# Kernel optimization log

Hardware: AMD Instinct MI355X
Metric: run time of the kernel (lower is better)

Reference implementation:

```python
import jax, jax.numpy as jnp
import numpy as np

# dims: batch, tokens, channels, heads, head_dim, slices, context_slices, context_dim
B, N, C, H, D, G, SC, DC = 2, 32768, 256, 8, 32, 32, 64, 32
EPS_SLICE = 1e-5


def _ln(x, g, b):
    m = x.mean(-1, keepdims=True)
    v = ((x - m) ** 2).mean(-1, keepdims=True)
    return (x - m) * jax.lax.rsqrt(v + 1e-5) * g + b


def setup_inputs() -> dict:
    key = jax.random.key(0)
    ks = jax.random.split(key, 16)
    w = lambda k, s: jax.random.normal(k, s, jnp.float32) * 0.02
    return dict(
        fx=jax.random.normal(ks[0], (B, N, C), jnp.float32),
        context=jax.random.normal(ks[1], (B, H, SC, DC), jnp.float32),
        ln1_g=jnp.ones((C,), jnp.float32), ln1_b=jnp.zeros((C,), jnp.float32),
        Wfx=w(ks[2], (C, H * D)), bfx=jnp.zeros((H * D,), jnp.float32),
        Wx=w(ks[3], (C, H * D)), bx=jnp.zeros((H * D,), jnp.float32),
        Wslice=w(ks[4], (D, G)), bslice=jnp.zeros((G,), jnp.float32),
        temperature=0.5 * jnp.ones((1, H, 1, 1), jnp.float32),
        Wq=w(ks[5], (D, D)), Wk=w(ks[6], (D, D)), Wv=w(ks[7], (D, D)),
        Wcq=w(ks[8], (D, D)), bcq=jnp.zeros((D,), jnp.float32),
        Wck=w(ks[9], (DC, D)), bck=jnp.zeros((D,), jnp.float32),
        Wcv=w(ks[10], (DC, D)), bcv=jnp.zeros((D,), jnp.float32),
        state_mixing=jnp.zeros((), jnp.float32),
        Wout=w(ks[11], (H * D, C)), bout=jnp.zeros((C,), jnp.float32),
        ln2_g=jnp.ones((C,), jnp.float32), ln2_b=jnp.zeros((C,), jnp.float32),
        Wm1=w(ks[12], (C, 4 * C)), bm1=jnp.zeros((4 * C,), jnp.float32),
        Wm2=w(ks[13], (4 * C, C)), bm2=jnp.zeros((C,), jnp.float32),
    )


def reference(fx, context, ln1_g, ln1_b, Wfx, bfx, Wx, bx, Wslice, bslice,
              temperature, Wq, Wk, Wv, Wcq, bcq, Wck, bck, Wcv, bcv,
              state_mixing, Wout, bout, ln2_g, ln2_b, Wm1, bm1, Wm2, bm2):
    # --- GALE attention on pre-normed input (Transolver physics attention + cross) ---
    x = _ln(fx, ln1_g, ln1_b)
    fxm = (x @ Wfx + bfx).reshape(B, N, H, D).transpose(0, 2, 1, 3)  # b h n d
    xm = (x @ Wx + bx).reshape(B, N, H, D).transpose(0, 2, 1, 3)    # b h n d
    # slice weights: softmax over slices with learnable per-head temperature
    sw = jax.nn.softmax((xm @ Wslice + bslice) / temperature, axis=-1)  # b h n g
    norm = sw.sum(2)  # b h g
    st = jnp.einsum('bhnd,bhng->bhgd', fxm, sw) / (norm + EPS_SLICE)[..., None]
    scale = D ** -0.5
    # self-attention among slice tokens (no bias on q/k/v)
    q, k, v = st @ Wq, st @ Wk, st @ Wv
    sattn = jax.nn.softmax(jnp.einsum('bhgd,bhmd->bhgm', q, k) * scale, axis=-1)
    self_tok = jnp.einsum('bhgm,bhmd->bhgd', sattn, v)
    # cross-attention of slice tokens onto geometry/global context
    cq = st @ Wcq + bcq
    ck = context @ Wck + bck
    cv = context @ Wcv + bcv
    cattn = jax.nn.softmax(jnp.einsum('bhgd,bhsd->bhgs', cq, ck) * scale, axis=-1)
    cross_tok = jnp.einsum('bhgs,bhsd->bhgd', cattn, cv)
    # sigmoid-gated mix
    mw = jax.nn.sigmoid(state_mixing)
    ost = mw * self_tok + (1.0 - mw) * cross_tok
    # de-slice back to tokens and output-project
    out = jnp.einsum('bhgd,bhng->bhnd', ost, sw)
    out = out.transpose(0, 2, 1, 3).reshape(B, N, H * D) @ Wout + bout
    fx = fx + out  # residual 1
    # --- MLP block ---
    h = _ln(fx, ln2_g, ln2_b)
    fx = fx + (jax.nn.gelu(h @ Wm1 + bm1, approximate=False) @ Wm2 + bm2)
    return fx
```

## Files before the change

kernel.cpp:

```cpp
#include <hip/hip_runtime.h>
#include <hip/hip_bf16.h>

#define BATCH 2
#define NTOK  32768
#define CH    256
#define NH    8
#define HDIM  32
#define NG    32
#define NSC   64
#define NDC   32

typedef __attribute__((ext_vector_type(8))) short short8v;
typedef __attribute__((ext_vector_type(4))) short short4v;
typedef __attribute__((ext_vector_type(4))) float f32x4;

static __device__ __forceinline__ short f2bf(float f) {
    __hip_bfloat16 h = __float2bfloat16(f);
    return __builtin_bit_cast(short, h);
}
static __device__ __forceinline__ float bf2f(short s) {
    return __bfloat162float(__builtin_bit_cast(__hip_bfloat16, s));
}

__global__ __launch_bounds__(256) void kconv_transpose(
    const float* __restrict__ in, __hip_bfloat16* __restrict__ out,
    int K, int N)
{
    __shared__ float t[32][33];
    const int nb = N >> 5;
    const int bk = blockIdx.x / nb;
    const int bn = blockIdx.x % nb;
    const int c = threadIdx.x & 31, r0 = threadIdx.x >> 5;
    #pragma unroll
    for (int i = 0; i < 4; ++i) {
        const int r = r0 + i * 8;
        t[r][c] = in[(long)(bk * 32 + r) * N + bn * 32 + c];
    }
    __syncthreads();
    #pragma unroll
    for (int i = 0; i < 4; ++i) {
        const int r = r0 + i * 8;
        out[(long)(bn * 32 + r) * K + bk * 32 + c] = __float2bfloat16(t[c][r]);
    }
}

__global__ __launch_bounds__(256) void kcomb(
    const float* __restrict__ Wx, const float* __restrict__ bx,
    const float* __restrict__ Wsl, const float* __restrict__ bsl,
    __hip_bfloat16* __restrict__ wcat2, float* __restrict__ bcomb)
{
    __shared__ float wcol[32];
    const int hc = blockIdx.x;
    const int h = hc >> 5, g = hc & 31;
    const int tid = threadIdx.x;
    if (tid < 32) wcol[tid] = Wsl[tid * 32 + g];
    __syncthreads();
    float a = 0.f;
    #pragma unroll
    for (int d = 0; d < 32; ++d) a += Wx[tid * 256 + h * 32 + d] * wcol[d];
    wcat2[(long)hc * 256 + tid] = __float2bfloat16(a);
    if (tid == 0) {
        float s = bsl[g];
        #pragma unroll
        for (int d = 0; d < 32; ++d) s += bx[h * 32 + d] * wcol[d];
        bcomb[hc] = s;
    }
}

__global__ __launch_bounds__(256, 2) void k1_mfma(
    const float* __restrict__ fx,
    const float* __restrict__ g1, const float* __restrict__ b1,
    const __hip_bfloat16* __restrict__ wcat,
    const float* __restrict__ bfx, const float* __restrict__ bcomb,
    const float* __restrict__ temp,
    __hip_bfloat16* __restrict__ fxm_o, __hip_bfloat16* __restrict__ sw_o)
{
    __shared__ __align__(16) char lds[65536];
    const int tid = threadIdx.x;
    const int lane = tid & 63, wid = tid >> 6;
    const long tok0 = (long)blockIdx.x * 64;
    const int col = lane & 15, kq = lane >> 4;
    const int swz = (col & 7) << 4;
    const int ep = ((kq * 16) ^ swz) & 48;
    const int e0 = (swz & 64) | ep;
    const int e1 = ((swz & 64) ^ 64) | ep;
    const int ab0 = col * 512 + e0, ab1 = col * 512 + e1;

    {
        const float4 gv = *reinterpret_cast<const float4*>(g1 + lane * 4);
        const float4 bv = *reinterpret_cast<const float4*>(b1 + lane * 4);
        for (int tt = 0; tt < 16; ++tt) {
            const int r = wid * 16 + tt;
            const float4 v = *reinterpret_cast<const float4*>(fx + (tok0 + r) * 256 + lane * 4);
            float s = v.x + v.y + v.z + v.w;
            float s2 = v.x * v.x + v.y * v.y + v.z * v.z + v.w * v.w;
            #pragma unroll
            for (int off = 32; off; off >>= 1) {
                s  += __shfl_xor(s,  off);
                s2 += __shfl_xor(s2, off);
            }
            const float mean = s * (1.f / 256.f);
            const float rs = rsqrtf(s2 * (1.f / 256.f) - mean * mean + 1e-5f);
            short4v o;
            o[0] = f2bf((v.x - mean) * rs * gv.x + bv.x);
            o[1] = f2bf((v.y - mean) * rs * gv.y + bv.y);
            o[2] = f2bf((v.z - mean) * rs * gv.z + bv.z);
            o[3] = f2bf((v.w - mean) * rs * gv.w + bv.w);
            const int addr = r * 512 + ((lane * 8) ^ ((r & 7) << 4));
            *reinterpret_cast<short4v*>(lds + addr) = o;
        }
    }
    __syncthreads();

    f32x4 acc[4][8];
    #pragma unroll
    for (int mt = 0; mt < 4; ++mt)
        #pragma unroll
        for (int nt = 0; nt < 8; ++nt) acc[mt][nt] = (f32x4){0.f, 0.f, 0.f, 0.f};

    const short* wp = reinterpret_cast<const short*>(wcat) + (wid * 128 + col) * 256 + kq * 8;
    #pragma unroll 2
    for (int j = 0; j < 4; ++j) {
        short8v a0[4], a1[4];
        #pragma unroll
        for (int mt = 0; mt < 4; ++mt) {
            a0[mt] = *reinterpret_cast<const short8v*>(lds + mt * 8192 + j * 128 + ab0);
            a1[mt] = *reinterpret_cast<const short8v*>(lds + mt * 8192 + j * 128 + ab1);
        }
        #pragma unroll
        for (int nt = 0; nt < 8; ++nt) {
            const short8v b0 = *reinterpret_cast<const short8v*>(wp + nt * 4096 + j * 64);
            const short8v b1 = *reinterpret_cast<const short8v*>(wp + nt * 4096 + j * 64 + 32);
            #pragma unroll
            for (int mt = 0; mt < 4; ++mt) {
                acc[mt][nt] = __builtin_amdgcn_mfma_f32_16x16x32_bf16(a0[mt], b0, acc[mt][nt], 0, 0, 0);
                acc[mt][nt] = __builtin_amdgcn_mfma_f32_16x16x32_bf16(a1[mt], b1, acc[mt][nt], 0, 0, 0);
            }
        }
    }
    __syncthreads();

    #pragma unroll
    for (int nt = 0; nt < 8; ++nt) {
        const int c = wid * 128 + nt * 16 + col;
        const float bb = (c < 256) ? bfx[c] : bcomb[c - 256];
        #pragma unroll
        for (int mt = 0; mt < 4; ++mt) {
            #pragma unroll
            for (int r = 0; r < 4; ++r) {
                const int row = mt * 16 + kq * 4 + r;
                const int byte = row * 1024 + ((c * 2) ^ ((row & 7) << 4));
                *reinterpret_cast<short*>(lds + byte) = f2bf(acc[mt][nt][r] + bb);
            }
        }
    }
    __syncthreads();

    #pragma unroll
    for (int it = 0; it < 8; ++it) {
        const int idx = it * 256 + tid;
        const int row = idx >> 5, ch = idx & 31;
        const short8v val = *reinterpret_cast<const short8v*>(
            lds + row * 1024 + ((ch * 16) ^ ((row & 7) << 4)));
        *reinterpret_cast<short8v*>(
            reinterpret_cast<short*>(fxm_o) + (tok0 + row) * 256 + ch * 8) = val;
    }

    #pragma unroll
    for (int pp = 0; pp < 2; ++pp) {
        const int p = pp * 256 + tid;
        const int t = p >> 3, h = p & 7;
        const float it_ = 1.f / temp[h];
        float lg[32];
        #pragma unroll
        for (int g = 0; g < 32; ++g) {
            const int byte = t * 1024 + (((256 + h * 32 + g) * 2) ^ ((t & 7) << 4));
            lg[g] = bf2f(*reinterpret_cast<const short*>(lds + byte)) * it_;
        }
        float mx = -1e30f;
        #pragma unroll
        for (int g = 0; g < 32; ++g) mx = fmaxf(mx, lg[g]);
        float ssum = 0.f;
        #pragma unroll
        for (int g = 0; g < 32; ++g) { lg[g] = __expf(lg[g] - mx); ssum += lg[g]; }
        const float inv = 1.f / ssum;
        #pragma unroll
        for (int g = 0; g < 32; ++g) {
            const int byte = t * 1024 + (((256 + h * 32 + g) * 2) ^ ((t & 7) << 4));
            *reinterpret_cast<short*>(lds + byte) = f2bf(lg[g] * inv);
        }
    }
    __syncthreads();

    #pragma unroll
    for (int it = 0; it < 8; ++it) {
        const int idx = it * 256 + tid;
        const int row = idx >> 5, ch = idx & 31;
        const short8v val = *reinterpret_cast<const short8v*>(
            lds + row * 1024 + ((512 + ch * 16) ^ ((row & 7) << 4)));
        *reinterpret_cast<short8v*>(
            reinterpret_cast<short*>(sw_o) + (tok0 + row) * 256 + ch * 8) = val;
    }
}

__global__ __launch_bounds__(256) void k2_st_partial(
    const __hip_bfloat16* __restrict__ fxm, const __hip_bfloat16* __restrict__ sw,
    float* __restrict__ pst, float* __restrict__ pn)
{
    __shared__ float fl[32][32];
    __shared__ float sl[32][32];
    const int tid = threadIdx.x;
    const int blk = blockIdx.x;
    const int bh = blk >> 5, chunk = blk & 31;
    const int b = bh >> 3, h = bh & 7;
    const long nbase = (long)b * NTOK + (long)chunk * 1024;
    const int g = tid >> 3, dq = tid & 7, db = dq * 4;
    const int lr = tid >> 3, lc4 = (tid & 7) * 4;
    float a0 = 0.f, a1 = 0.f, a2 = 0.f, a3 = 0.f, nacc = 0.f;

    for (int nb = 0; nb < 1024; nb += 32) {
        const long base = (nbase + nb + lr) * 256 + h * 32 + lc4;
        const short4v fv = *reinterpret_cast<const short4v*>(
            reinterpret_cast<const short*>(fxm) + base);
        const short4v sv = *reinterpret_cast<const short4v*>(
            reinterpret_cast<const short*>(sw) + base);
        float4 ff, sf;
        ff.x = bf2f(fv[0]); ff.y = bf2f(fv[1]); ff.z = bf2f(fv[2]); ff.w = bf2f(fv[3]);
        sf.x = bf2f(sv[0]); sf.y = bf2f(sv[1]); sf.z = bf2f(sv[2]); sf.w = bf2f(sv[3]);
        __syncthreads();
        *reinterpret_cast<float4*>(&fl[lr][lc4]) = ff;
        *reinterpret_cast<float4*>(&sl[lr][lc4]) = sf;
        __syncthreads();
        #pragma unroll
        for (int t = 0; t < 32; ++t) {
            const float s = sl[t][g];
            if (dq == 0) nacc += s;
            a0 += s * fl[t][db + 0];
            a1 += s * fl[t][db + 1];
            a2 += s * fl[t][db + 2];
            a3 += s * fl[t][db + 3];
        }
    }
    float* o = pst + (long)blk * 1024 + g * 32 + db;
    o[0] = a0; o[1] = a1; o[2] = a2; o[3] = a3;
    if (dq == 0) pn[blk * 32 + g] = nacc;
}

__global__ __launch_bounds__(256) void k3_slice_attn(
    const float* __restrict__ pst, const float* __restrict__ pn,
    const float* __restrict__ ctx,
    const float* __restrict__ Wq, const float* __restrict__ Wk, const float* __restrict__ Wv,
    const float* __restrict__ Wcq, const float* __restrict__ bcq,
    const float* __restrict__ Wck, const float* __restrict__ bck,
    const float* __restrict__ Wcv, const float* __restrict__ bcv,
    const float* __restrict__ mix, __hip_bfloat16* __restrict__ ostT_o)
{
    __shared__ float st[1024], qm[1024], km[1024], vm[1024], cqm[1024];
    __shared__ float ckm[2048], cvm[2048], attn[2048], stok[1024], nb[32];
    const int tid = threadIdx.x;
    const int bh = blockIdx.x;

    if (tid < 32) {
        float s = 0.f;
        for (int c = 0; c < 32; ++c) s += pn[(bh * 32 + c) * 32 + tid];
        nb[tid] = s;
    }
    __syncthreads();
    for (int i = tid; i < 1024; i += 256) {
        float s = 0.f;
        for (int c = 0; c < 32; ++c) s += pst[(long)(bh * 32 + c) * 1024 + i];
        st[i] = s / (nb[i >> 5] + 1e-5f);
    }
    __syncthreads();

    for (int i = tid; i < 1024; i += 256) {
        const int g = i >> 5, d = i & 31;
        float aq = 0.f, ak = 0.f, av = 0.f, ac = bcq[d];
        #pragma unroll
        for (int e = 0; e < 32; ++e) {
            const float s = st[g * 32 + e];
            aq += s * Wq[e * 32 + d];
            ak += s * Wk[e * 32 + d];
            av += s * Wv[e * 32 + d];
            ac += s * Wcq[e * 32 + d];
        }
        qm[i] = aq; km[i] = ak; vm[i] = av; cqm[i] = ac;
    }
    const float* cbp = ctx + (long)bh * (NSC * NDC);
    for (int i = tid; i < 2048; i += 256) {
        const int s_ = i >> 5, d = i & 31;
        float w1 = bck[d], w2 = bcv[d];
        #pragma unroll
        for (int e = 0; e < 32; ++e) {
            const float cval = cbp[s_ * 32 + e];
            w1 += cval * Wck[e * 32 + d];
            w2 += cval * Wcv[e * 32 + d];
        }
        ckm[i] = w1; cvm[i] = w2;
    }
    __syncthreads();

    const float scale = 0.17677669529663687f;
    for (int i = tid; i < 1024; i += 256) {
        const int g = i >> 5, m = i & 31;
        float a = 0.f;
        #pragma unroll
        for (int d = 0; d < 32; ++d) a += qm[g * 32 + d] * km[m * 32 + d];
        attn[i] = a * scale;
    }
    __syncthreads();
    if (tid < 32) {
        float mx = -1e30f;
        for (int m = 0; m < 32; ++m) mx = fmaxf(mx, attn[tid * 32 + m]);
        float s = 0.f;
        for (int m = 0; m < 32; ++m) { const float e = expf(attn[tid * 32 + m] - mx); attn[tid * 32 + m] = e; s += e; }
        const float inv = 1.f / s;
        for (int m = 0; m < 32; ++m) attn[tid * 32 + m] *= inv;
    }
    __syncthreads();
    for (int i = tid; i < 1024; i += 256) {
        const int g = i >> 5, d = i & 31;
        float a = 0.f;
        #pragma unroll
        for (int m = 0; m < 32; ++m) a += attn[g * 32 + m] * vm[m * 32 + d];
        stok[i] = a;
    }
    __syncthreads();
    for (int i = tid; i < 2048; i += 256) {
        const int g = i >> 6, s_ = i & 63;
        float a = 0.f;
        #pragma unroll
        for (int d = 0; d < 32; ++d) a += cqm[g * 32 + d] * ckm[s_ * 32 + d];
        attn[i] = a * scale;
    }
    __syncthreads();
    if (tid < 32) {
        float mx = -1e30f;
        for (int m = 0; m < 64; ++m) mx = fmaxf(mx, attn[tid * 64 + m]);
        float s = 0.f;
        for (int m = 0; m < 64; ++m) { const float e = expf(attn[tid * 64 + m] - mx); attn[tid * 64 + m] = e; s += e; }
        const float inv = 1.f / s;
        for (int m = 0; m < 64; ++m) attn[tid * 64 + m] *= inv;
    }
    __syncthreads();
    const float mw = 1.f / (1.f + expf(-mix[0]));
    for (int i = tid; i < 1024; i += 256) {
        const int g = i >> 5, d = i & 31;
        float a = 0.f;
        #pragma unroll
        for (int s_ = 0; s_ < 64; ++s_) a += attn[g * 64 + s_] * cvm[s_ * 32 + d];
        const float val = mw * stok[i] + (1.f - mw) * a;
        ostT_o[(long)bh * 1024 + d * 32 + g] = __float2bfloat16(val);
    }
}

__global__ __launch_bounds__(256, 2) void k4_mfma(
    const __hip_bfloat16* __restrict__ sw, const __hip_bfloat16* __restrict__ ostT,
    const __hip_bfloat16* __restrict__ woutt, const float* __restrict__ bout,
    const float* __restrict__ fx, float* __restrict__ out)
{
    __shared__ __align__(16) char lds[65536];
    const int tid = threadIdx.x;
    const int lane = tid & 63, wid = tid >> 6;
    const long tok0 = (long)blockIdx.x * 64;
    const int b = (int)(tok0 >> 15);
    const int col = lane & 15, kq = lane >> 4;
    const int swz = (col & 7) << 4;
    const int ep = ((kq * 16) ^ swz) & 48;
    const int e0 = (swz & 64) | ep;
    const int e1 = ((swz & 64) ^ 64) | ep;
    const int ab0 = col * 512 + e0, ab1 = col * 512 + e1;

    #pragma unroll
    for (int it = 0; it < 8; ++it) {
        const int idx = it * 256 + tid;
        const int row = idx >> 5, ch = idx & 31;
        const short8v val = *reinterpret_cast<const short8v*>(
            reinterpret_cast<const short*>(sw) + (tok0 + row) * 256 + ch * 8);
        *reinterpret_cast<short8v*>(lds + row * 512 + ((ch * 16) ^ ((row & 7) << 4))) = val;
    }
    __syncthreads();

    f32x4 accal[2][4][2];
    #pragma unroll
    for (int hh = 0; hh < 2; ++hh) {
        const int h = wid * 2 + hh;
        short8v a[4];
        #pragma unroll
        for (int mt = 0; mt < 4; ++mt)
            a[mt] = *reinterpret_cast<const short8v*>(
                lds + mt * 8192 + wid * 128 + (hh ? ab1 : ab0));
        #pragma unroll
        for (int nt = 0; nt < 2; ++nt) {
            const int d = nt * 16 + col;
            const short8v bfr = *reinterpret_cast<const short8v*>(
                reinterpret_cast<const short*>(ostT) + ((b * 8 + h) * 32 + d) * 32 + kq * 8);
            #pragma unroll
            for (int mt = 0; mt < 4; ++mt) {
                accal[hh][mt][nt] = (f32x4){0.f, 0.f, 0.f, 0.f};
                accal[hh][mt][nt] = __builtin_amdgcn_mfma_f32_16x16x32_bf16(
                    a[mt], bfr, accal[hh][mt][nt], 0, 0, 0);
            }
        }
    }
    #pragma unroll
    for (int hh = 0; hh < 2; ++hh) {
        const int h = wid * 2 + hh;
        #pragma unroll
        for (int nt = 0; nt < 2; ++nt) {
            const int cc = h * 32 + nt * 16 + col;
            #pragma unroll
            for (int mt = 0; mt < 4; ++mt) {
                #pragma unroll
                for (int r = 0; r < 4; ++r) {
                    const int row = mt * 16 + kq * 4 + r;
                    const int byte = 32768 + row * 512 + ((cc * 2) ^ ((row & 7) << 4));
                    *reinterpret_cast<short*>(lds + byte) = f2bf(accal[hh][mt][nt][r]);
                }
            }
        }
    }
    __syncthreads();

    f32x4 acc[4][4];
    #pragma unroll
    for (int mt = 0; mt < 4; ++mt)
        #pragma unroll
        for (int nt = 0; nt < 4; ++nt) acc[mt][nt] = (f32x4){0.f, 0.f, 0.f, 0.f};

    const short* wp = reinterpret_cast<const short*>(woutt) + (wid * 64 + col) * 256 + kq * 8;
    #pragma unroll 2
    for (int j = 0; j < 4; ++j) {
        short8v a0[4], a1[4];
        #pragma unroll
        for (int mt = 0; mt < 4; ++mt) {
            a0[mt] = *reinterpret_cast<const short8v*>(lds + 32768 + mt * 8192 + j * 128 + ab0);
            a1[mt] = *reinterpret_cast<const short8v*>(lds + 32768 + mt * 8192 + j * 128 + ab1);
        }
        #pragma unroll
        for (int nt = 0; nt < 4; ++nt) {
            const short8v b0 = *reinterpret_cast<const short8v*>(wp + nt * 4096 + j * 64);
            const short8v b1 = *reinterpret_cast<const short8v*>(wp + nt * 4096 + j * 64 + 32);
            #pragma unroll
            for (int mt = 0; mt < 4; ++mt) {
                acc[mt][nt] = __builtin_amdgcn_mfma_f32_16x16x32_bf16(a0[mt], b0, acc[mt][nt], 0, 0, 0);
                acc[mt][nt] = __builtin_amdgcn_mfma_f32_16x16x32_bf16(a1[mt], b1, acc[mt][nt], 0, 0, 0);
            }
        }
    }

    #pragma unroll
    for (int nt = 0; nt < 4; ++nt) {
        const int c = wid * 64 + nt * 16 + col;
        const float bb = bout[c];
        #pragma unroll
        for (int mt = 0; mt < 4; ++mt) {
            #pragma unroll
            for (int r = 0; r < 4; ++r) {
                const int row = mt * 16 + kq * 4 + r;
                const long idx = (tok0 + row) * 256 + c;
                out[idx] = acc[mt][nt][r] + bb + fx[idx];
            }
        }
    }
}

__global__ __launch_bounds__(512, 4) void k5_mlp_mfma(
    float* __restrict__ io,
    const float* __restrict__ g2, const float* __restrict__ b2,
    const __hip_bfloat16* __restrict__ w1t, const float* __restrict__ bm1,
    const __hip_bfloat16* __restrict__ w2t, const float* __restrict__ bm2)
{
    __shared__ __align__(16) char lds[65536];
    const int tid = threadIdx.x;
    const int lane = tid & 63, wid = tid >> 6;
    const long tok0 = (long)blockIdx.x * 64;
    const int col = lane & 15, kq = lane >> 4;
    const int n0 = wid * 32;
    const int swz = (col & 7) << 4;
    const int ep = ((kq * 16) ^ swz) & 48;
    const int e0 = (swz & 64) | ep;
    const int e1 = ((swz & 64) ^ 64) | ep;
    const int ab0 = col * 512 + e0, ab1 = col * 512 + e1;

    {
        const float4 gv = *reinterpret_cast<const float4*>(g2 + lane * 4);
        const float4 bv = *reinterpret_cast<const float4*>(b2 + lane * 4);
        #pragma unroll
        for (int tt = 0; tt < 8; ++tt) {
            const int r = wid * 8 + tt;
            const float4 v = *reinterpret_cast<const float4*>(io + (tok0 + r) * 256 + lane * 4);
            float s = v.x + v.y + v.z + v.w;
            float s2 = v.x * v.x + v.y * v.y + v.z * v.z + v.w * v.w;
            #pragma unroll
            for (int off = 32; off; off >>= 1) {
                s  += __shfl_xor(s,  off);
                s2 += __shfl_xor(s2, off);
            }
            const float mean = s * (1.f / 256.f);
            const float rs = rsqrtf(s2 * (1.f / 256.f) - mean * mean + 1e-5f);
            short4v o;
            o[0] = f2bf((v.x - mean) * rs * gv.x + bv.x);
            o[1] = f2bf((v.y - mean) * rs * gv.y + bv.y);
            o[2] = f2bf((v.z - mean) * rs * gv.z + bv.z);
            o[3] = f2bf((v.w - mean) * rs * gv.w + bv.w);
            const int addr = r * 512 + ((lane * 8) ^ ((r & 7) << 4));
            *reinterpret_cast<short4v*>(lds + addr) = o;
        }
    }
    __syncthreads();

    const short* w1s = reinterpret_cast<const short*>(w1t) + (n0 + col) * 256 + kq * 8;
    const short* w2s = reinterpret_cast<const short*>(w2t) + (n0 + col) * 1024 + kq * 8;
    const int gsw = (kq & 1) << 6;

    f32x4 accO[4][2];
    #pragma unroll
    for (int mt = 0; mt < 4; ++mt)
        #pragma unroll
        for (int nt = 0; nt < 2; ++nt) accO[mt][nt] = (f32x4){0.f, 0.f, 0.f, 0.f};

    for (int ch = 0; ch < 4; ++ch) {
        f32x4 accP[4][2];
        #pragma unroll
        for (int mt = 0; mt < 4; ++mt)
            #pragma unroll
            for (int nt = 0; nt < 2; ++nt) accP[mt][nt] = (f32x4){0.f, 0.f, 0.f, 0.f};

        #pragma unroll 2
        for (int j = 0; j < 4; ++j) {
            short8v a0[4], a1[4];
            #pragma unroll
            for (int mt = 0; mt < 4; ++mt) {
                a0[mt] = *reinterpret_cast<const short8v*>(lds + mt * 8192 + j * 128 + ab0);
                a1[mt] = *reinterpret_cast<const short8v*>(lds + mt * 8192 + j * 128 + ab1);
            }
            #pragma unroll
            for (int nt = 0; nt < 2; ++nt) {
                const short8v b0 = *reinterpret_cast<const short8v*>(
                    w1s + ch * 65536 + nt * 4096 + j * 64);
                const short8v b1 = *reinterpret_cast<const short8v*>(
                    w1s + ch * 65536 + nt * 4096 + j * 64 + 32);
                #pragma unroll
                for (int mt = 0; mt < 4; ++mt) {
                    accP[mt][nt] = __builtin_amdgcn_mfma_f32_16x16x32_bf16(a0[mt], b0, accP[mt][nt], 0, 0, 0);
                    accP[mt][nt] = __builtin_amdgcn_mfma_f32_16x16x32_bf16(a1[mt], b1, accP[mt][nt], 0, 0, 0);
                }
            }
        }

        __syncthreads();
        #pragma unroll
        for (int nt = 0; nt < 2; ++nt) {
            const float b1v = bm1[ch * 256 + n0 + nt * 16 + col];
            const int k2i2 = (n0 + nt * 16 + col) * 2;
            #pragma unroll
            for (int mt = 0; mt < 4; ++mt) {
                #pragma unroll
                for (int r = 0; r < 4; ++r) {
                    float m = accP[mt][nt][r] + b1v;
                    const float u = __builtin_fmaf(0.044715f * m, m * m, m);
                    const float e = __expf(-1.5957691216057308f * u);
                    m = m * __builtin_amdgcn_rcpf(1.f + e);
                    const int byte = 32768 + kq * 2048 + mt * 8192 + r * 512
                                     + (k2i2 ^ (gsw + r * 16));
                    *reinterpret_cast<short*>(lds + byte) = f2bf(m);
                }
            }
        }
        __syncthreads();

        #pragma unroll 2
        for (int j = 0; j < 4; ++j) {
            short8v a0[4], a1[4];
            #pragma unroll
            for (int mt = 0; mt < 4; ++mt) {
                a0[mt] = *reinterpret_cast<const short8v*>(lds + 32768 + mt * 8192 + j * 128 + ab0);
                a1[mt] = *reinterpret_cast<const short8v*>(lds + 32768 + mt * 8192 + j * 128 + ab1);
            }
            #pragma unroll
            for (int nt = 0; nt < 2; ++nt) {
                const short8v b0 = *reinterpret_cast<const short8v*>(
                    w2s + nt * 16384 + ch * 256 + j * 64);
                const short8v b1 = *reinterpret_cast<const short8v*>(
                    w2s + nt * 16384 + ch * 256 + j * 64 + 32);
                #pragma unroll
                for (int mt = 0; mt < 4; ++mt) {
                    accO[mt][nt] = __builtin_amdgcn_mfma_f32_16x16x32_bf16(a0[mt], b0, accO[mt][nt], 0, 0, 0);
                    accO[mt][nt] = __builtin_amdgcn_mfma_f32_16x16x32_bf16(a1[mt], b1, accO[mt][nt], 0, 0, 0);
                }
            }
        }
    }

    #pragma unroll
    for (int nt = 0; nt < 2; ++nt) {
        const int c = n0 + nt * 16 + col;
        const float b2v = bm2[c];
        #pragma unroll
        for (int mt = 0; mt < 4; ++mt) {
            #pragma unroll
            for (int r = 0; r < 4; ++r) {
                const int row = mt * 16 + kq * 4 + r;
                const long idx = (tok0 + row) * 256 + c;
                io[idx] = io[idx] + accO[mt][nt][r] + b2v;
            }
        }
    }
}

extern "C" void kernel_launch(void* const* d_in, const int* in_sizes, int n_in,
                              void* d_out, int out_size, void* d_ws, size_t ws_size,
                              hipStream_t stream)
{
    const float* fx   = (const float*)d_in[0];
    const float* ctx  = (const float*)d_in[1];
    const float* g1   = (const float*)d_in[2];
    const float* b1   = (const float*)d_in[3];
    const float* Wfx  = (const float*)d_in[4];
    const float* bfx  = (const float*)d_in[5];
    const float* Wx   = (const float*)d_in[6];
    const float* bx   = (const float*)d_in[7];
    const float* Wsl  = (const float*)d_in[8];
    const float* bsl  = (const float*)d_in[9];
    const float* temp = (const float*)d_in[10];
    const float* Wq   = (const float*)d_in[11];
    const float* Wk   = (const float*)d_in[12];
    const float* Wv   = (const float*)d_in[13];
    const float* Wcq  = (const float*)d_in[14];
    const float* bcq  = (const float*)d_in[15];
    const float* Wck  = (const float*)d_in[16];
    const float* bck  = (const float*)d_in[17];
    const float* Wcv  = (const float*)d_in[18];
    const float* bcv  = (const float*)d_in[19];
    const float* mix  = (const float*)d_in[20];
    const float* Wout = (const float*)d_in[21];
    const float* bout = (const float*)d_in[22];
    const float* g2   = (const float*)d_in[23];
    const float* b2   = (const float*)d_in[24];
    const float* Wm1  = (const float*)d_in[25];
    const float* bm1  = (const float*)d_in[26];
    const float* Wm2  = (const float*)d_in[27];
    const float* bm2  = (const float*)d_in[28];
    float* out = (float*)d_out;

    char* ws = (char*)d_ws;
    __hip_bfloat16* fxm  = (__hip_bfloat16*)ws;
    __hip_bfloat16* sw   = (__hip_bfloat16*)(ws + (size_t)33554432);
    float* pst = (float*)(ws + (size_t)67108864);
    float* pn  = (float*)(ws + (size_t)69206016);
    __hip_bfloat16* ostT  = (__hip_bfloat16*)(ws + (size_t)69271552);
    __hip_bfloat16* wcat  = (__hip_bfloat16*)(ws + (size_t)69304320);
    __hip_bfloat16* woutt = (__hip_bfloat16*)(ws + (size_t)69566464);
    __hip_bfloat16* w1t   = (__hip_bfloat16*)(ws + (size_t)69697536);
    __hip_bfloat16* w2t   = (__hip_bfloat16*)(ws + (size_t)70221824);
    float* bcomb          = (float*)(ws + (size_t)70746112);

    kconv_transpose<<<64,  256, 0, stream>>>(Wfx, wcat,  256, 256);
    kcomb<<<256, 256, 0, stream>>>(Wx, bx, Wsl, bsl, wcat + 65536, bcomb);
    kconv_transpose<<<64,  256, 0, stream>>>(Wout, woutt, 256, 256);
    kconv_transpose<<<256, 256, 0, stream>>>(Wm1, w1t,    256, 1024);
    kconv_transpose<<<256, 256, 0, stream>>>(Wm2, w2t,    1024, 256);

    k1_mfma<<<1024, 256, 0, stream>>>(fx, g1, b1, wcat, bfx, bcomb, temp,
                                      fxm, sw);
    k2_st_partial<<<512, 256, 0, stream>>>(fxm, sw, pst, pn);
    k3_slice_attn<<<16, 256, 0, stream>>>(pst, pn, ctx, Wq, Wk, Wv,
                                          Wcq, bcq, Wck, bck, Wcv, bcv, mix, ostT);
    k4_mfma<<<1024, 256, 0, stream>>>(sw, ostT, woutt, bout, fx, out);
    k5_mlp_mfma<<<1024, 512, 0, stream>>>(out, g2, b2, w1t, bm1, w2t, bm2);
}
```

Measured before the change: 334.7 us.

## Rewrite slice reduction, stage epilogues through LDS, software-pipeline MLP GEMMs

The slice-token reduction kernel now has each wave accumulate a 4x4 register tile over its own 256-token range with direct global loads, then combines the four waves' partials through shared memory. This removes the per-step double barrier and LDS round trip. The output-projection and MLP epilogues now stage results in LDS and write the residual add with coalesced float4 accesses instead of strided scalar global stores. The MLP loop is restructured so the second GEMM for chunk ch runs interleaved with the first GEMM for chunk ch+1, overlapping the two MFMA streams at the cost of more live accumulators and register pressure.

```diff
diff --git a/kernel.cpp b/kernel.cpp
--- a/kernel.cpp
+++ b/kernel.cpp
@@ -207,43 +207,57 @@
     const __hip_bfloat16* __restrict__ fxm, const __hip_bfloat16* __restrict__ sw,
     float* __restrict__ pst, float* __restrict__ pn)
 {
-    __shared__ float fl[32][32];
-    __shared__ float sl[32][32];
-    const int tid = threadIdx.x;
+    __shared__ float psum[4][32][32];
+    __shared__ float pns[4][32];
+    const int tid = threadIdx.x, wid = tid >> 6, lane = tid & 63;
     const int blk = blockIdx.x;
     const int bh = blk >> 5, chunk = blk & 31;
     const int b = bh >> 3, h = bh & 7;
-    const long nbase = (long)b * NTOK + (long)chunk * 1024;
-    const int g = tid >> 3, dq = tid & 7, db = dq * 4;
-    const int lr = tid >> 3, lc4 = (tid & 7) * 4;
-    float a0 = 0.f, a1 = 0.f, a2 = 0.f, a3 = 0.f, nacc = 0.f;
-
-    for (int nb = 0; nb < 1024; nb += 32) {
-        const long base = (nbase + nb + lr) * 256 + h * 32 + lc4;
-        const short4v fv = *reinterpret_cast<const short4v*>(
-            reinterpret_cast<const short*>(fxm) + base);
-        const short4v sv = *reinterpret_cast<const short4v*>(
-            reinterpret_cast<const short*>(sw) + base);
-        float4 ff, sf;
-        ff.x = bf2f(fv[0]); ff.y = bf2f(fv[1]); ff.z = bf2f(fv[2]); ff.w = bf2f(fv[3]);
-        sf.x = bf2f(sv[0]); sf.y = bf2f(sv[1]); sf.z = bf2f(sv[2]); sf.w = bf2f(sv[3]);
-        __syncthreads();
-        *reinterpret_cast<float4*>(&fl[lr][lc4]) = ff;
-        *reinterpret_cast<float4*>(&sl[lr][lc4]) = sf;
-        __syncthreads();
-        #pragma unroll
-        for (int t = 0; t < 32; ++t) {
-            const float s = sl[t][g];
-            if (dq == 0) nacc += s;
-            a0 += s * fl[t][db + 0];
-            a1 += s * fl[t][db + 1];
-            a2 += s * fl[t][db + 2];
-            a3 += s * fl[t][db + 3];
-        }
-    }
-    float* o = pst + (long)blk * 1024 + g * 32 + db;
-    o[0] = a0; o[1] = a1; o[2] = a2; o[3] = a3;
-    if (dq == 0) pn[blk * 32 + g] = nacc;
+    const long rbase = (long)b * NTOK + (long)chunk * 1024 + wid * 256;
+    const int gB = lane >> 3, dB = lane & 7;
+    const short* sp = reinterpret_cast<const short*>(sw) + rbase * 256 + h * 32 + gB * 4;
+    const short* fp = reinterpret_cast<const short*>(fxm) + rbase * 256 + h * 32 + dB * 4;
+
+    float acc[4][4];
+    float nacc[4];
+    #pragma unroll
+    for (int i = 0; i < 4; ++i) {
+        nacc[i] = 0.f;
+        #pragma unroll
+        for (int j = 0; j < 4; ++j) acc[i][j] = 0.f;
+    }
+
+    #pragma unroll 4
+    for (int r = 0; r < 256; ++r) {
+        const short4v s4 = *reinterpret_cast<const short4v*>(sp + r * 256);
+        const short4v f4 = *reinterpret_cast<const short4v*>(fp + r * 256);
+        float sg[4], fd[4];
+        #pragma unroll
+        for (int i = 0; i < 4; ++i) { sg[i] = bf2f(s4[i]); fd[i] = bf2f(f4[i]); }
+        #pragma unroll
+        for (int gg = 0; gg < 4; ++gg) {
+            nacc[gg] += sg[gg];
+            #pragma unroll
+            for (int dd = 0; dd < 4; ++dd) acc[gg][dd] += sg[gg] * fd[dd];
+        }
+    }
+
+    #pragma unroll
+    for (int gg = 0; gg < 4; ++gg) {
+        #pragma unroll
+        for (int dd = 0; dd < 4; ++dd)
+            psum[wid][gB * 4 + gg][dB * 4 + dd] = acc[gg][dd];
+        if (dB == 0) pns[wid][gB * 4 + gg] = nacc[gg];
+    }
+    __syncthreads();
+
+    for (int i = tid; i < 1024; i += 256) {
+        const int g = i >> 5, d = i & 31;
+        pst[(long)blk * 1024 + i] =
+            psum[0][g][d] + psum[1][g][d] + psum[2][g][d] + psum[3][g][d];
+    }
+    if (tid < 32)
+        pn[blk * 32 + tid] = pns[0][tid] + pns[1][tid] + pns[2][tid] + pns[3][tid];
 }
 
 __global__ __launch_bounds__(256) void k3_slice_attn(
@@ -449,6 +463,8 @@
         }
     }
 
+    __syncthreads();
+    float* lf = reinterpret_cast<float*>(lds);
     #pragma unroll
     for (int nt = 0; nt < 4; ++nt) {
         const int c = wid * 64 + nt * 16 + col;
@@ -458,10 +474,21 @@
             #pragma unroll
             for (int r = 0; r < 4; ++r) {
                 const int row = mt * 16 + kq * 4 + r;
-                const long idx = (tok0 + row) * 256 + c;
-                out[idx] = acc[mt][nt][r] + bb + fx[idx];
-            }
-        }
+                lf[row * 256 + c] = acc[mt][nt][r] + bb;
+            }
+        }
+    }
+    __syncthreads();
+    #pragma unroll
+    for (int it = 0; it < 16; ++it) {
+        const int q = it * 256 + tid;
+        const int row = q >> 6, c4 = (q & 63) * 4;
+        const float4 v = *reinterpret_cast<const float4*>(lf + row * 256 + c4);
+        const long gidx = (tok0 + row) * 256 + c4;
+        const float4 f = *reinterpret_cast<const float4*>(fx + gidx);
+        float4 o;
+        o.x = v.x + f.x; o.y = v.y + f.y; o.z = v.z + f.z; o.w = v.w + f.w;
+        *reinterpret_cast<float4*>(out + gidx) = o;
     }
 }
 
@@ -514,41 +541,36 @@
     const short* w2s = reinterpret_cast<const short*>(w2t) + (n0 + col) * 1024 + kq * 8;
     const int gsw = (kq & 1) << 6;
 
-    f32x4 accO[4][2];
+    f32x4 accP[4][2], accO[4][2];
     #pragma unroll
     for (int mt = 0; mt < 4; ++mt)
         #pragma unroll
-        for (int nt = 0; nt < 2; ++nt) accO[mt][nt] = (f32x4){0.f, 0.f, 0.f, 0.f};
+        for (int nt = 0; nt < 2; ++nt) {
+            accP[mt][nt] = (f32x4){0.f, 0.f, 0.f, 0.f};
+            accO[mt][nt] = (f32x4){0.f, 0.f, 0.f, 0.f};
+        }
+
+    #pragma unroll 1
+    for (int j = 0; j < 4; ++j) {
+        short8v b0[2], b1[2];
+        #pragma unroll
+        for (int nt = 0; nt < 2; ++nt) {
+            b0[nt] = *reinterpret_cast<const short8v*>(w1s + nt * 4096 + j * 64);
+            b1[nt] = *reinterpret_cast<const short8v*>(w1s + nt * 4096 + j * 64 + 32);
+        }
+        #pragma unroll
+        for (int mt = 0; mt < 4; ++mt) {
+            const short8v a0 = *reinterpret_cast<const short8v*>(lds + mt * 8192 + j * 128 + ab0);
+            const short8v a1 = *reinterpret_cast<const short8v*>(lds + mt * 8192 + j * 128 + ab1);
+            #pragma unroll
+            for (int nt = 0; nt < 2; ++nt) {
+                accP[mt][nt] = __builtin_amdgcn_mfma_f32_16x16x32_bf16(a0, b0[nt], accP[mt][nt], 0, 0, 0);
+                accP[mt][nt] = __builtin_amdgcn_mfma_f32_16x16x32_bf16(a1, b1[nt], accP[mt][nt], 0, 0, 0);
+            }
+        }
+    }
 
     for (int ch = 0; ch < 4; ++ch) {
-        f32x4 accP[4][2];
-        #pragma unroll
-        for (int mt = 0; mt < 4; ++mt)
-            #pragma unroll
-            for (int nt = 0; nt < 2; ++nt) accP[mt][nt] = (f32x4){0.f, 0.f, 0.f, 0.f};
-
-        #pragma unroll 2
-        for (int j = 0; j < 4; ++j) {
-            short8v a0[4], a1[4];
-            #pragma unroll
-            for (int mt = 0; mt < 4; ++mt) {
-                a0[mt] = *reinterpret_cast<const short8v*>(lds + mt * 8192 + j * 128 + ab0);
-                a1[mt] = *reinterpret_cast<const short8v*>(lds + mt * 8192 + j * 128 + ab1);
-            }
-            #pragma unroll
-            for (int nt = 0; nt < 2; ++nt) {
-                const short8v b0 = *reinterpret_cast<const short8v*>(
-                    w1s + ch * 65536 + nt * 4096 + j * 64);
-                const short8v b1 = *reinterpret_cast<const short8v*>(
-                    w1s + ch * 65536 + nt * 4096 + j * 64 + 32);
-                #pragma unroll
-                for (int mt = 0; mt < 4; ++mt) {
-                    accP[mt][nt] = __builtin_amdgcn_mfma_f32_16x16x32_bf16(a0[mt], b0, accP[mt][nt], 0, 0, 0);
-                    accP[mt][nt] = __builtin_amdgcn_mfma_f32_16x16x32_bf16(a1[mt], b1, accP[mt][nt], 0, 0, 0);
-                }
-            }
-        }
-
         __syncthreads();
         #pragma unroll
         for (int nt = 0; nt < 2; ++nt) {
@@ -570,42 +592,93 @@
         }
         __syncthreads();
 
-        #pragma unroll 2
-        for (int j = 0; j < 4; ++j) {
-            short8v a0[4], a1[4];
-            #pragma unroll
-            for (int mt = 0; mt < 4; ++mt) {
-                a0[mt] = *reinterpret_cast<const short8v*>(lds + 32768 + mt * 8192 + j * 128 + ab0);
-                a1[mt] = *reinterpret_cast<const short8v*>(lds + 32768 + mt * 8192 + j * 128 + ab1);
-            }
-            #pragma unroll
-            for (int nt = 0; nt < 2; ++nt) {
-                const short8v b0 = *reinterpret_cast<const short8v*>(
-                    w2s + nt * 16384 + ch * 256 + j * 64);
-                const short8v b1 = *reinterpret_cast<const short8v*>(
-                    w2s + nt * 16384 + ch * 256 + j * 64 + 32);
+        if (ch < 3) {
+            #pragma unroll
+            for (int mt = 0; mt < 4; ++mt)
+                #pragma unroll
+                for (int nt = 0; nt < 2; ++nt) accP[mt][nt] = (f32x4){0.f, 0.f, 0.f, 0.f};
+
+            #pragma unroll 1
+            for (int j = 0; j < 4; ++j) {
+                short8v b20[2], b21[2], b10[2], b11[2];
+                #pragma unroll
+                for (int nt = 0; nt < 2; ++nt) {
+                    b20[nt] = *reinterpret_cast<const short8v*>(w2s + nt * 16384 + ch * 256 + j * 64);
+                    b21[nt] = *reinterpret_cast<const short8v*>(w2s + nt * 16384 + ch * 256 + j * 64 + 32);
+                    b10[nt] = *reinterpret_cast<const short8v*>(w1s + (ch + 1) * 65536 + nt * 4096 + j * 64);
+                    b11[nt] = *reinterpret_cast<const short8v*>(w1s + (ch + 1) * 65536 + nt * 4096 + j * 64 + 32);
+                }
                 #pragma unroll
                 for (int mt = 0; mt < 4; ++mt) {
-                    accO[mt][nt] = __builtin_amdgcn_mfma_f32_16x16x32_bf16(a0[mt], b0, accO[mt][nt], 0, 0, 0);
-                    accO[mt][nt] = __builtin_amdgcn_mfma_f32_16x16x32_bf16(a1[mt], b1, accO[mt][nt], 0, 0, 0);
+                    const short8v x0 = *reinterpret_cast<const short8v*>(lds + 32768 + mt * 8192 + j * 128 + ab0);
+                    const short8v x1 = *reinterpret_cast<const short8v*>(lds + 32768 + mt * 8192 + j * 128 + ab1);
+                    const short8v y0 = *reinterpret_cast<const short8v*>(lds + mt * 8192 + j * 128 + ab0);
+                    const short8v y1 = *reinterpret_cast<const short8v*>(lds + mt * 8192 + j * 128 + ab1);
+                    #pragma unroll
+                    for (int nt = 0; nt < 2; ++nt) {
+                        accO[mt][nt] = __builtin_amdgcn_mfma_f32_16x16x32_bf16(x0, b20[nt], accO[mt][nt], 0, 0, 0);
+                        accO[mt][nt] = __builtin_amdgcn_mfma_f32_16x16x32_bf16(x1, b21[nt], accO[mt][nt], 0, 0, 0);
+                        accP[mt][nt] = __builtin_amdgcn_mfma_f32_16x16x32_bf16(y0, b10[nt], accP[mt][nt], 0, 0, 0);
+                        accP[mt][nt] = __builtin_amdgcn_mfma_f32_16x16x32_bf16(y1, b11[nt], accP[mt][nt], 0, 0, 0);
+                    }
                 }
             }
-        }
-    }
-
-    #pragma unroll
-    for (int nt = 0; nt < 2; ++nt) {
-        const int c = n0 + nt * 16 + col;
-        const float b2v = bm2[c];
-        #pragma unroll
-        for (int mt = 0; mt < 4; ++mt) {
-            #pragma unroll
-            for (int r = 0; r < 4; ++r) {
-                const int row = mt * 16 + kq * 4 + r;
-                const long idx = (tok0 + row) * 256 + c;
-                io[idx] = io[idx] + accO[mt][nt][r] + b2v;
-            }
-        }
+        } else {
+            #pragma unroll 1
+            for (int j = 0; j < 4; ++j) {
+                short8v b20[2], b21[2];
+                #pragma unroll
+                for (int nt = 0; nt < 2; ++nt) {
+                    b20[nt] = *reinterpret_cast<const short8v*>(w2s + nt * 16384 + 3 * 256 + j * 64);
+                    b21[nt] = *reinterpret_cast<const short8v*>(w2s + nt * 16384 + 3 * 256 + j * 64 + 32);
+                }
+                #pragma unroll
+                for (int mt = 0; mt < 4; ++mt) {
+                    const short8v x0 = *reinterpret_cast<const short8v*>(lds + 32768 + mt * 8192 + j * 128 + ab0);
+                    const short8v x1 = *reinterpret_cast<const short8v*>(lds + 32768 + mt * 8192 + j * 128 + ab1);
+                    #pragma unroll
+                    for (int nt = 0; nt < 2; ++nt) {
+                        accO[mt][nt] = __builtin_amdgcn_mfma_f32_16x16x32_bf16(x0, b20[nt], accO[mt][nt], 0, 0, 0);
+                        accO[mt][nt] = __builtin_amdgcn_mfma_f32_16x16x32_bf16(x1, b21[nt], accO[mt][nt], 0, 0, 0);
+                    }
+                }
+            }
+        }
+    }
+
+    __syncthreads();
+    float* lf = reinterpret_cast<float*>(lds);
+    #pragma unroll
+    for (int half = 0; half < 2; ++half) {
+        if ((wid >> 2) == half) {
+            #pragma unroll
+            for (int nt = 0; nt < 2; ++nt) {
+                const int c = n0 + nt * 16 + col;
+                const float b2v = bm2[c];
+                const int cl = c - half * 128;
+                #pragma unroll
+                for (int mt = 0; mt < 4; ++mt) {
+                    #pragma unroll
+                    for (int r = 0; r < 4; ++r) {
+                        const int row = mt * 16 + kq * 4 + r;
+                        lf[row * 128 + cl] = accO[mt][nt][r] + b2v;
+                    }
+                }
+            }
+        }
+        __syncthreads();
+        #pragma unroll
+        for (int it = 0; it < 4; ++it) {
+            const int q = it * 512 + tid;
+            const int row = q >> 5, c4 = (q & 31) * 4;
+            const float4 v = *reinterpret_cast<const float4*>(lf + row * 128 + c4);
+            const long gidx = (tok0 + row) * 256 + half * 128 + c4;
+            const float4 f = *reinterpret_cast<const float4*>(io + gidx);
+            float4 o;
+            o.x = v.x + f.x; o.y = v.y + f.y; o.z = v.z + f.z; o.w = v.w + f.w;
+            *reinterpret_cast<float4*>(io + gidx) = o;
+        }
+        __syncthreads();
     }
 }
 
```

New measurement: 422.6 us. 1.26x slower.
